# Performance work log

Hardware: AMD Instinct MI355X
Metric: run time of the kernel (lower is better)

## Reference

```python
import jax, jax.numpy as jnp
import numpy as np

NUM_NODES = 10000
NUM_EDGES = 160000
IN_CH = 768
TYPE_DIM = 128
HID = 768
OUT = 768
NUM_REL = 3
NUM_NODE_TYPE = 3


def _glorot(key, shape):
    fan_in, fan_out = shape[-2], shape[-1]
    lim = (6.0 / (fan_in + fan_out)) ** 0.5
    return jax.random.uniform(key, shape, jnp.float32, -lim, lim)


def setup_inputs() -> dict:
    key = jax.random.key(0)
    ks = jax.random.split(key, 16)
    d1 = IN_CH + TYPE_DIM  # 896
    inp = {
        "x": jax.random.normal(ks[0], (NUM_NODES, IN_CH), jnp.float32),
        "node_type": jax.random.randint(ks[1], (NUM_NODES,), 0, NUM_NODE_TYPE, jnp.int32),
        "edge_index": jax.random.randint(ks[2], (2, NUM_EDGES), 0, NUM_NODES, jnp.int32),
        "edge_type": jax.random.randint(ks[3], (NUM_EDGES,), 0, NUM_REL, jnp.int32),
        "node_emb": jax.random.normal(ks[4], (NUM_NODE_TYPE, TYPE_DIM), jnp.float32),
        # layer 1: d1 -> d1
        "w_rel1": _glorot(ks[5], (NUM_REL, d1, d1)),
        "w_root1": _glorot(ks[6], (d1, d1)),
        "b1": jnp.zeros((d1,), jnp.float32),
        # layer 2: d1 -> HID
        "w_rel2": _glorot(ks[7], (NUM_REL, d1, HID)),
        "w_root2": _glorot(ks[8], (d1, HID)),
        "b2": jnp.zeros((HID,), jnp.float32),
        # layer 3: HID -> OUT
        "w_rel3": _glorot(ks[9], (NUM_REL, HID, OUT)),
        "w_root3": _glorot(ks[10], (HID, OUT)),
        "b3": jnp.zeros((OUT,), jnp.float32),
    }
    return inp


def rgcn_conv(h, src, dst, edge_type, w_rel, w_root, bias):
    """PyG-style RGCNConv: per-relation linear + per-relation mean aggregation at dst."""
    num_nodes = h.shape[0]
    # per-relation transforms of all nodes: [R, N, out]
    xw = jnp.einsum('nd,rde->rne', h, w_rel)
    # gather the message for each edge according to its relation: [E, out]
    msg = xw[edge_type, src]
    # per-(node, relation) incoming-edge counts for mean aggregation
    onehot = jax.nn.one_hot(edge_type, NUM_REL, dtype=h.dtype)        # [E, R]
    count = jax.ops.segment_sum(onehot, dst, num_segments=num_nodes)  # [N, R]
    inv = jnp.where(count > 0, 1.0 / jnp.maximum(count, 1.0), 0.0)
    msg = msg * inv[dst, edge_type][:, None]
    agg = jax.ops.segment_sum(msg, dst, num_segments=num_nodes)       # [N, out]
    return agg + h @ w_root + bias


def reference(x, node_type, edge_index, edge_type, node_emb,
              w_rel1, w_root1, b1, w_rel2, w_root2, b2, w_rel3, w_root3, b3):
    src, dst = edge_index[0], edge_index[1]
    h = jnp.concatenate([x, node_emb[node_type]], axis=-1)  # [N, 896]
    h = jax.nn.relu(rgcn_conv(h, src, dst, edge_type, w_rel1, w_root1, b1))
    h = jax.nn.relu(rgcn_conv(h, src, dst, edge_type, w_rel2, w_root2, b2))
    h = jax.nn.relu(rgcn_conv(h, src, dst, edge_type, w_rel3, w_root3, b3))
    return h
```

## Files before the change

### kernel.cpp

```cpp
#include <hip/hip_runtime.h>
#include <stdint.h>
#include <stddef.h>

#define N_NODES 10000
#define N_EDGES 160000
#define IN_CH   768
#define TYPE_DIM 128
#define D1      896
#define HID     768
#define N_REL   3
#define NB      (N_NODES * N_REL)

typedef _Float16 f16;
typedef _Float16 f16x4 __attribute__((ext_vector_type(4)));
typedef _Float16 f16x8 __attribute__((ext_vector_type(8)));
typedef float    f32x4 __attribute__((ext_vector_type(4)));

__global__ void prep_kernel(const float* __restrict__ x, const int* __restrict__ node_type,
                            const float* __restrict__ node_emb, f16* __restrict__ H,
                            int* __restrict__ counts) {
    int bid = blockIdx.x;
    if (bid < 235) {
        int i = bid * 256 + threadIdx.x;
        if (i < 2 * NB) counts[i] = 0;
        return;
    }
    int tid = (bid - 235) * 256 + threadIdx.x;
    int n = tid / (D1 / 4);
    int c = (tid % (D1 / 4)) * 4;
    if (n >= N_NODES) return;
    float4 v;
    if (c < IN_CH) v = *(const float4*)(x + (size_t)n * IN_CH + c);
    else           v = *(const float4*)(node_emb + (size_t)node_type[n] * TYPE_DIM + (c - IN_CH));
    f16x4 o; o[0] = (f16)v.x; o[1] = (f16)v.y; o[2] = (f16)v.z; o[3] = (f16)v.w;
    *(f16x4*)(H + (size_t)n * D1 + c) = o;
}

__global__ void count_kernel(const int* __restrict__ ei, const int* __restrict__ et,
                             int* __restrict__ counts) {
    int e = blockIdx.x * 256 + threadIdx.x;
    if (e >= N_EDGES) return;
    atomicAdd(&counts[ei[N_EDGES + e] * N_REL + et[e]], 1);
}

__global__ void scan_kernel(const int* __restrict__ counts, int* __restrict__ row_ptr) {
    __shared__ int part[1024];
    int t = threadIdx.x;
    const int CH = (NB + 1023) / 1024;
    int s = 0;
    for (int i = 0; i < CH; i++) { int idx = t * CH + i; if (idx < NB) s += counts[idx]; }
    part[t] = s;
    __syncthreads();
    for (int off = 1; off < 1024; off <<= 1) {
        int v = part[t];
        int u = (t >= off) ? part[t - off] : 0;
        __syncthreads();
        part[t] = v + u;
        __syncthreads();
    }
    int base = (t > 0) ? part[t - 1] : 0;
    for (int i = 0; i < CH; i++) {
        int idx = t * CH + i;
        if (idx < NB) { row_ptr[idx] = base; base += counts[idx]; }
    }
    if (t == 1023) row_ptr[NB] = base;
}

__global__ void fill_kernel(const int* __restrict__ ei, const int* __restrict__ et,
                            const int* __restrict__ row_ptr, int* __restrict__ cursor,
                            int* __restrict__ entries) {
    int e = blockIdx.x * 256 + threadIdx.x;
    if (e >= N_EDGES) return;
    int b = ei[N_EDGES + e] * N_REL + et[e];
    int pos = atomicAdd(&cursor[b], 1);
    entries[row_ptr[b] + pos] = ei[e];
}

__global__ void transpose_all(const float* __restrict__ w1, const float* __restrict__ w2,
                              const float* __restrict__ w3, const float* __restrict__ w4,
                              const float* __restrict__ w5, const float* __restrict__ w6,
                              f16* __restrict__ bt1, f16* __restrict__ bt2,
                              f16* __restrict__ bt3) {
    __shared__ float t[32][33];
    int bid = blockIdx.x;
    const float* w; f16* bt; int N, ldbt, koff, KB;
    if (bid < 2352)      {             w = w1; N = 896; bt = bt1; ldbt = 3584; koff = 0;    KB = 84; }
    else if (bid < 3136) { bid -= 2352; w = w2; N = 896; bt = bt1; ldbt = 3584; koff = 2688; KB = 28; }
    else if (bid < 5152) { bid -= 3136; w = w3; N = 768; bt = bt2; ldbt = 3584; koff = 0;    KB = 84; }
    else if (bid < 5824) { bid -= 5152; w = w4; N = 768; bt = bt2; ldbt = 3584; koff = 2688; KB = 28; }
    else if (bid < 7552) { bid -= 5824; w = w5; N = 768; bt = bt3; ldbt = 3072; koff = 0;    KB = 72; }
    else                 { bid -= 7552; w = w6; N = 768; bt = bt3; ldbt = 3072; koff = 2304; KB = 24; }
    int kb = (bid % KB) * 32, nb = (bid / KB) * 32;
    int tx = threadIdx.x, ty = threadIdx.y;
#pragma unroll
    for (int i = 0; i < 4; i++)
        t[ty * 4 + i][tx] = w[(size_t)(kb + ty * 4 + i) * N + nb + tx];
    __syncthreads();
#pragma unroll
    for (int i = 0; i < 4; i++)
        bt[(size_t)(nb + ty * 4 + i) * ldbt + koff + kb + tx] = (f16)t[tx][ty * 4 + i];
}

template <int DIN>
__global__ __launch_bounds__(256) void aggregate_wave(
    const f16* __restrict__ h, const int* __restrict__ row_ptr,
    const int* __restrict__ entries, f16* __restrict__ out, const int ldout) {
    const int b = blockIdx.x * 4 + (threadIdx.x >> 6);
    const int lane = threadIdx.x & 63;
    constexpr int C2 = DIN / 8 - 64;
    const int beg = row_ptr[b], end = row_ptr[b + 1];
    float a0[8], a1[8];
#pragma unroll
    for (int i = 0; i < 8; i++) { a0[i] = 0.f; a1[i] = 0.f; }
    int e = beg;
    for (; e + 4 <= end; e += 4) {
        const f16* rA = h + (size_t)entries[e] * DIN;
        const f16* rB = h + (size_t)entries[e + 1] * DIN;
        const f16* rC = h + (size_t)entries[e + 2] * DIN;
        const f16* rD = h + (size_t)entries[e + 3] * DIN;
        f16x8 vA0 = *(const f16x8*)(rA + lane * 8);
        f16x8 vB0 = *(const f16x8*)(rB + lane * 8);
        f16x8 vC0 = *(const f16x8*)(rC + lane * 8);
        f16x8 vD0 = *(const f16x8*)(rD + lane * 8);
        if (lane < C2) {
            f16x8 vA1 = *(const f16x8*)(rA + 512 + lane * 8);
            f16x8 vB1 = *(const f16x8*)(rB + 512 + lane * 8);
            f16x8 vC1 = *(const f16x8*)(rC + 512 + lane * 8);
            f16x8 vD1 = *(const f16x8*)(rD + 512 + lane * 8);
#pragma unroll
            for (int i = 0; i < 8; i++)
                a1[i] += ((float)vA1[i] + (float)vB1[i]) + ((float)vC1[i] + (float)vD1[i]);
        }
#pragma unroll
        for (int i = 0; i < 8; i++)
            a0[i] += ((float)vA0[i] + (float)vB0[i]) + ((float)vC0[i] + (float)vD0[i]);
    }
    for (; e + 2 <= end; e += 2) {
        const f16* rA = h + (size_t)entries[e] * DIN;
        const f16* rB = h + (size_t)entries[e + 1] * DIN;
        f16x8 vA0 = *(const f16x8*)(rA + lane * 8);
        f16x8 vB0 = *(const f16x8*)(rB + lane * 8);
        if (lane < C2) {
            f16x8 vA1 = *(const f16x8*)(rA + 512 + lane * 8);
            f16x8 vB1 = *(const f16x8*)(rB + 512 + lane * 8);
#pragma unroll
            for (int i = 0; i < 8; i++) { a1[i] += (float)vA1[i]; a1[i] += (float)vB1[i]; }
        }
#pragma unroll
        for (int i = 0; i < 8; i++) { a0[i] += (float)vA0[i]; a0[i] += (float)vB0[i]; }
    }
    if (e < end) {
        const f16* rA = h + (size_t)entries[e] * DIN;
        f16x8 vA0 = *(const f16x8*)(rA + lane * 8);
        if (lane < C2) {
            f16x8 vA1 = *(const f16x8*)(rA + 512 + lane * 8);
#pragma unroll
            for (int i = 0; i < 8; i++) a1[i] += (float)vA1[i];
        }
#pragma unroll
        for (int i = 0; i < 8; i++) a0[i] += (float)vA0[i];
    }
    const float s = (end > beg) ? 1.0f / (float)(end - beg) : 0.f;
    f16* o = out + (size_t)(b / N_REL) * ldout + (size_t)(b % N_REL) * DIN;
    f16x8 w0, w1;
#pragma unroll
    for (int i = 0; i < 8; i++) { w0[i] = (f16)(a0[i] * s); w1[i] = (f16)(a1[i] * s); }
    *(f16x8*)(o + lane * 8) = w0;
    if (lane < C2) *(f16x8*)(o + 512 + lane * 8) = w1;
}

__device__ __forceinline__ void gload16(const void* g, void* l) {
    __builtin_amdgcn_global_load_lds(
        (const __attribute__((address_space(1))) unsigned int*)g,
        (__attribute__((address_space(3))) unsigned int*)l, 16, 0, 0);
}

__global__ __launch_bounds__(512, 4) void gemm_f16_ilv(
    const f16* __restrict__ A1, const int K1,
    const f16* __restrict__ A2, const int K2,
    const f16* __restrict__ BT, const int ldbt,
    const float* __restrict__ bias,
    const int M, const int N,
    f16* __restrict__ Cf16, const int ldc16, float* __restrict__ Cf32) {
    __shared__ f16 T[2 * 16384];

    const int CB = N >> 7;
    const int nwg = gridDim.x;
    const int q = nwg >> 3, r = nwg & 7;
    const int orig = blockIdx.x;
    const int xcd = orig & 7, pos = orig >> 3;
    const int wg = (xcd < r ? xcd * (q + 1) : r * (q + 1) + (xcd - r) * q) + pos;
    const int x = wg / CB, y = wg - x * CB;
    const int row0 = x * 128, col0 = y * 128;

    const int tid  = threadIdx.x;
    const int lane = tid & 63;
    const int wave = tid >> 6;
    const int wr = wave >> 2, wc = wave & 3;
    const int l16 = lane & 15, hi = lane >> 4;
    const int key = l16 & 7;
    const int pAf = (hi ^ key) * 8;
    const int pBf = ((4 | hi) ^ key) * 8;

    f32x4 acc[4][2];
#pragma unroll
    for (int m = 0; m < 4; m++)
#pragma unroll
        for (int n = 0; n < 2; n++) acc[m][n] = (f32x4){0.f, 0.f, 0.f, 0.f};

    const int r_  = tid >> 3;
    const int sl  = (tid & 7) ^ (r_ & 7);
    const bool isA = sl < 4;
    const int colA = sl * 8;
    const int colB = (sl - 4) * 8;
    const f16* pLo[2]; const f16* pHi[2];
#pragma unroll
    for (int j = 0; j < 2; j++) {
        const int rr = r_ + 64 * j;
        if (isA) {
            pLo[j] = A1 + (size_t)(row0 + rr) * K1 + colA;
            pHi[j] = A2 + (size_t)(row0 + rr) * K2 + colA - K1;
        } else {
            pLo[j] = BT + (size_t)(col0 + rr) * ldbt + colB;
            pHi[j] = pLo[j];
        }
    }

    const int KT = K1 + K2;
    const int nt = KT >> 6;

#define STAGE(t) do {                                                  \
        const int k0_ = (t) * 64;                                      \
        f16* l_ = T + ((t) & 1) * 16384 + tid * 8;                     \
        _Pragma("unroll")                                              \
        for (int j = 0; j < 2; j++) {                                  \
            const f16* s_ = ((k0_ < K1) ? pLo[j] : pHi[j]) + k0_;      \
            gload16(s_,      l_ + j * 4096);                           \
            gload16(s_ + 32, l_ + 8192 + j * 4096);                    \
        }                                                              \
    } while (0)

    STAGE(0);
    for (int t = 0; t < nt; ++t) {
        if (t + 1 < nt) {
            STAGE(t + 1);
            asm volatile("s_waitcnt vmcnt(4)" ::: "memory");
        } else {
            asm volatile("s_waitcnt vmcnt(0)" ::: "memory");
        }
        __builtin_amdgcn_s_barrier();

        const f16* Tb = T + (t & 1) * 16384;
        f16x8 af[2][4], bf[2][2];
#pragma unroll
        for (int h = 0; h < 2; h++) {
#pragma unroll
            for (int m = 0; m < 4; m++)
                af[h][m] = *(const f16x8*)(Tb + h * 8192 + (wr * 64 + m * 16 + l16) * 64 + pAf);
#pragma unroll
            for (int n = 0; n < 2; n++)
                bf[h][n] = *(const f16x8*)(Tb + h * 8192 + (wc * 32 + n * 16 + l16) * 64 + pBf);
        }
#pragma unroll
        for (int h = 0; h < 2; h++)
#pragma unroll
            for (int m = 0; m < 4; m++)
#pragma unroll
                for (int n = 0; n < 2; n++)
                    acc[m][n] = __builtin_amdgcn_mfma_f32_16x16x32_f16(af[h][m], bf[h][n], acc[m][n], 0, 0, 0);

        asm volatile("s_barrier" ::: "memory");
    }
#undef STAGE

    const int hi4 = hi * 4;
#pragma unroll
    for (int m = 0; m < 4; m++) {
#pragma unroll
        for (int n = 0; n < 2; n++) {
            const int col = col0 + wc * 32 + n * 16 + l16;
            const float bv = bias[col];
#pragma unroll
            for (int rr2 = 0; rr2 < 4; rr2++) {
                const int row = row0 + wr * 64 + m * 16 + hi4 + rr2;
                if (row < M) {
                    float v = acc[m][n][rr2] + bv;
                    v = v > 0.f ? v : 0.f;
                    if (Cf16) Cf16[(size_t)row * ldc16 + col] = (f16)v;
                    else      Cf32[(size_t)row * N + col] = v;
                }
            }
        }
    }
}

extern "C" void kernel_launch(void* const* d_in, const int* in_sizes, int n_in,
                              void* d_out, int out_size, void* d_ws, size_t ws_size,
                              hipStream_t stream) {
    const float* x         = (const float*)d_in[0];
    const int*   node_type = (const int*)d_in[1];
    const int*   ei        = (const int*)d_in[2];
    const int*   et        = (const int*)d_in[3];
    const float* node_emb  = (const float*)d_in[4];
    const float* w_rel1    = (const float*)d_in[5];
    const float* w_root1   = (const float*)d_in[6];
    const float* b1        = (const float*)d_in[7];
    const float* w_rel2    = (const float*)d_in[8];
    const float* w_root2   = (const float*)d_in[9];
    const float* b2        = (const float*)d_in[10];
    const float* w_rel3    = (const float*)d_in[11];
    const float* w_root3   = (const float*)d_in[12];
    const float* b3        = (const float*)d_in[13];

    char* ws = (char*)d_ws;
    f16* AGG = (f16*)(ws + 0);
    f16* Ha  = (f16*)(ws + 53760000);
    f16* Hb  = (f16*)(ws + 71680000);
    f16* BT1 = (f16*)(ws + 89600000);
    f16* BT2 = (f16*)(ws + 96022528);
    f16* BT3 = (f16*)(ws + 101527552);
    int* counts  = (int*)(ws + 106246144);
    int* cursor  = (int*)(ws + 106366144);
    int* row_ptr = (int*)(ws + 106486144);
    int* entries = (int*)(ws + 106606148);

    prep_kernel<<<235 + 8750, 256, 0, stream>>>(x, node_type, node_emb, Ha, counts);
    count_kernel<<<N_EDGES / 256, 256, 0, stream>>>(ei, et, counts);
    scan_kernel<<<1, 1024, 0, stream>>>(counts, row_ptr);
    fill_kernel<<<N_EDGES / 256, 256, 0, stream>>>(ei, et, row_ptr, cursor, entries);

    transpose_all<<<8128, dim3(32, 8), 0, stream>>>(w_rel1, w_root1, w_rel2, w_root2,
                                                    w_rel3, w_root3, BT1, BT2, BT3);

    const int RB = (N_NODES + 127) / 128;

    aggregate_wave<D1><<<NB / 4, 256, 0, stream>>>(Ha, row_ptr, entries, AGG, 2688);
    gemm_f16_ilv<<<RB * 7, 512, 0, stream>>>(AGG, 2688, Ha, 896, BT1, 3584, b1,
                                             N_NODES, 896, Hb, 896, nullptr);
    aggregate_wave<D1><<<NB / 4, 256, 0, stream>>>(Hb, row_ptr, entries, AGG, 2688);
    gemm_f16_ilv<<<RB * 6, 512, 0, stream>>>(AGG, 2688, Hb, 896, BT2, 3584, b2,
                                             N_NODES, 768, Ha, 768, nullptr);
    aggregate_wave<HID><<<NB / 4, 256, 0, stream>>>(Ha, row_ptr, entries, AGG, 2304);
    gemm_f16_ilv<<<RB * 6, 512, 0, stream>>>(AGG, 2304, Ha, 768, BT3, 3072, b3,
                                             N_NODES, 768, nullptr, 0, (float*)d_out);
}
```

Before: 414.2 us.

## Fuse scan, feature prep and weight transpose into one launch; drop cursor array

The exclusive scan, the f16 feature conversion and the weight transpose now run as block ranges of a single kernel, so the serial single-block scan overlaps with the bulk conversion work instead of running as its own launch. The fill step increments row_ptr atomically in place, removing the separate cursor array and its zeroing. Aggregation then reads each segment's start from the previous entry. The scan block shrinks from 1024 to 256 threads, so each thread walks more elements serially.

New measurement: 425.5 us. +2.7%, slower.

```diff
diff --git a/kernel.cpp b/kernel.cpp
--- a/kernel.cpp
+++ b/kernel.cpp
@@ -16,24 +16,9 @@
 typedef _Float16 f16x8 __attribute__((ext_vector_type(8)));
 typedef float    f32x4 __attribute__((ext_vector_type(4)));
 
-__global__ void prep_kernel(const float* __restrict__ x, const int* __restrict__ node_type,
-                            const float* __restrict__ node_emb, f16* __restrict__ H,
-                            int* __restrict__ counts) {
-    int bid = blockIdx.x;
-    if (bid < 235) {
-        int i = bid * 256 + threadIdx.x;
-        if (i < 2 * NB) counts[i] = 0;
-        return;
-    }
-    int tid = (bid - 235) * 256 + threadIdx.x;
-    int n = tid / (D1 / 4);
-    int c = (tid % (D1 / 4)) * 4;
-    if (n >= N_NODES) return;
-    float4 v;
-    if (c < IN_CH) v = *(const float4*)(x + (size_t)n * IN_CH + c);
-    else           v = *(const float4*)(node_emb + (size_t)node_type[n] * TYPE_DIM + (c - IN_CH));
-    f16x4 o; o[0] = (f16)v.x; o[1] = (f16)v.y; o[2] = (f16)v.z; o[3] = (f16)v.w;
-    *(f16x4*)(H + (size_t)n * D1 + c) = o;
+__global__ void zero_counts(int* __restrict__ a) {
+    int i = blockIdx.x * 256 + threadIdx.x;
+    if (i < NB) a[i] = 0;
 }
 
 __global__ void count_kernel(const int* __restrict__ ei, const int* __restrict__ et,
@@ -43,46 +28,51 @@
     atomicAdd(&counts[ei[N_EDGES + e] * N_REL + et[e]], 1);
 }
 
-__global__ void scan_kernel(const int* __restrict__ counts, int* __restrict__ row_ptr) {
-    __shared__ int part[1024];
-    int t = threadIdx.x;
-    const int CH = (NB + 1023) / 1024;
-    int s = 0;
-    for (int i = 0; i < CH; i++) { int idx = t * CH + i; if (idx < NB) s += counts[idx]; }
-    part[t] = s;
-    __syncthreads();
-    for (int off = 1; off < 1024; off <<= 1) {
-        int v = part[t];
-        int u = (t >= off) ? part[t - off] : 0;
+__global__ void mega_prep(const int* __restrict__ counts, int* __restrict__ row_ptr,
+                          const float* __restrict__ x, const int* __restrict__ node_type,
+                          const float* __restrict__ node_emb, f16* __restrict__ H,
+                          const float* __restrict__ w1, const float* __restrict__ w2,
+                          const float* __restrict__ w3, const float* __restrict__ w4,
+                          const float* __restrict__ w5, const float* __restrict__ w6,
+                          f16* __restrict__ bt1, f16* __restrict__ bt2,
+                          f16* __restrict__ bt3) {
+    int bid = blockIdx.x;
+    if (bid == 0) {
+        __shared__ int part[256];
+        int t = threadIdx.x;
+        const int CH = (NB + 255) / 256;
+        int s = 0;
+        for (int i = 0; i < CH; i++) { int idx = t * CH + i; if (idx < NB) s += counts[idx]; }
+        part[t] = s;
         __syncthreads();
-        part[t] = v + u;
-        __syncthreads();
-    }
-    int base = (t > 0) ? part[t - 1] : 0;
-    for (int i = 0; i < CH; i++) {
-        int idx = t * CH + i;
-        if (idx < NB) { row_ptr[idx] = base; base += counts[idx]; }
-    }
-    if (t == 1023) row_ptr[NB] = base;
-}
-
-__global__ void fill_kernel(const int* __restrict__ ei, const int* __restrict__ et,
-                            const int* __restrict__ row_ptr, int* __restrict__ cursor,
-                            int* __restrict__ entries) {
-    int e = blockIdx.x * 256 + threadIdx.x;
-    if (e >= N_EDGES) return;
-    int b = ei[N_EDGES + e] * N_REL + et[e];
-    int pos = atomicAdd(&cursor[b], 1);
-    entries[row_ptr[b] + pos] = ei[e];
-}
-
-__global__ void transpose_all(const float* __restrict__ w1, const float* __restrict__ w2,
-                              const float* __restrict__ w3, const float* __restrict__ w4,
-                              const float* __restrict__ w5, const float* __restrict__ w6,
-                              f16* __restrict__ bt1, f16* __restrict__ bt2,
-                              f16* __restrict__ bt3) {
-    __shared__ float t[32][33];
-    int bid = blockIdx.x;
+        for (int off = 1; off < 256; off <<= 1) {
+            int v = part[t];
+            int u = (t >= off) ? part[t - off] : 0;
+            __syncthreads();
+            part[t] = v + u;
+            __syncthreads();
+        }
+        int base = (t > 0) ? part[t - 1] : 0;
+        for (int i = 0; i < CH; i++) {
+            int idx = t * CH + i;
+            if (idx < NB) { row_ptr[idx] = base; base += counts[idx]; }
+        }
+        return;
+    }
+    if (bid < 1 + 8750) {
+        int tid = (bid - 1) * 256 + threadIdx.x;
+        int n = tid / (D1 / 4);
+        int c = (tid % (D1 / 4)) * 4;
+        if (n >= N_NODES) return;
+        float4 v;
+        if (c < IN_CH) v = *(const float4*)(x + (size_t)n * IN_CH + c);
+        else           v = *(const float4*)(node_emb + (size_t)node_type[n] * TYPE_DIM + (c - IN_CH));
+        f16x4 o; o[0] = (f16)v.x; o[1] = (f16)v.y; o[2] = (f16)v.z; o[3] = (f16)v.w;
+        *(f16x4*)(H + (size_t)n * D1 + c) = o;
+        return;
+    }
+    __shared__ float tbuf[32][33];
+    bid -= 8751;
     const float* w; f16* bt; int N, ldbt, koff, KB;
     if (bid < 2352)      {             w = w1; N = 896; bt = bt1; ldbt = 3584; koff = 0;    KB = 84; }
     else if (bid < 3136) { bid -= 2352; w = w2; N = 896; bt = bt1; ldbt = 3584; koff = 2688; KB = 28; }
@@ -91,14 +81,23 @@
     else if (bid < 7552) { bid -= 5824; w = w5; N = 768; bt = bt3; ldbt = 3072; koff = 0;    KB = 72; }
     else                 { bid -= 7552; w = w6; N = 768; bt = bt3; ldbt = 3072; koff = 2304; KB = 24; }
     int kb = (bid % KB) * 32, nb = (bid / KB) * 32;
-    int tx = threadIdx.x, ty = threadIdx.y;
+    int tx = threadIdx.x & 31, ty = threadIdx.x >> 5;
 #pragma unroll
     for (int i = 0; i < 4; i++)
-        t[ty * 4 + i][tx] = w[(size_t)(kb + ty * 4 + i) * N + nb + tx];
+        tbuf[ty * 4 + i][tx] = w[(size_t)(kb + ty * 4 + i) * N + nb + tx];
     __syncthreads();
 #pragma unroll
     for (int i = 0; i < 4; i++)
-        bt[(size_t)(nb + ty * 4 + i) * ldbt + koff + kb + tx] = (f16)t[tx][ty * 4 + i];
+        bt[(size_t)(nb + ty * 4 + i) * ldbt + koff + kb + tx] = (f16)tbuf[tx][ty * 4 + i];
+}
+
+__global__ void fill_kernel(const int* __restrict__ ei, const int* __restrict__ et,
+                            int* __restrict__ row_ptr, int* __restrict__ entries) {
+    int e = blockIdx.x * 256 + threadIdx.x;
+    if (e >= N_EDGES) return;
+    int b = ei[N_EDGES + e] * N_REL + et[e];
+    int pos = atomicAdd(&row_ptr[b], 1);
+    entries[pos] = ei[e];
 }
 
 template <int DIN>
@@ -108,7 +107,8 @@
     const int b = blockIdx.x * 4 + (threadIdx.x >> 6);
     const int lane = threadIdx.x & 63;
     constexpr int C2 = DIN / 8 - 64;
-    const int beg = row_ptr[b], end = row_ptr[b + 1];
+    const int beg = (b > 0) ? row_ptr[b - 1] : 0;
+    const int end = row_ptr[b];
     float a0[8], a1[8];
 #pragma unroll
     for (int i = 0; i < 8; i++) { a0[i] = 0.f; a1[i] = 0.f; }
@@ -320,17 +320,16 @@
     f16* BT2 = (f16*)(ws + 96022528);
     f16* BT3 = (f16*)(ws + 101527552);
     int* counts  = (int*)(ws + 106246144);
-    int* cursor  = (int*)(ws + 106366144);
-    int* row_ptr = (int*)(ws + 106486144);
-    int* entries = (int*)(ws + 106606148);
-
-    prep_kernel<<<235 + 8750, 256, 0, stream>>>(x, node_type, node_emb, Ha, counts);
+    int* row_ptr = (int*)(ws + 106366144);
+    int* entries = (int*)(ws + 106486148);
+
+    zero_counts<<<(NB + 255) / 256, 256, 0, stream>>>(counts);
     count_kernel<<<N_EDGES / 256, 256, 0, stream>>>(ei, et, counts);
-    scan_kernel<<<1, 1024, 0, stream>>>(counts, row_ptr);
-    fill_kernel<<<N_EDGES / 256, 256, 0, stream>>>(ei, et, row_ptr, cursor, entries);
-
-    transpose_all<<<8128, dim3(32, 8), 0, stream>>>(w_rel1, w_root1, w_rel2, w_root2,
-                                                    w_rel3, w_root3, BT1, BT2, BT3);
+    mega_prep<<<1 + 8750 + 8128, 256, 0, stream>>>(counts, row_ptr,
+                                                   x, node_type, node_emb, Ha,
+                                                   w_rel1, w_root1, w_rel2, w_root2,
+                                                   w_rel3, w_root3, BT1, BT2, BT3);
+    fill_kernel<<<N_EDGES / 256, 256, 0, stream>>>(ei, et, row_ptr, entries);
 
     const int RB = (N_NODES + 127) / 128;
 
```
